# Optimization experiments

Measured on AMD Instinct MI355X. Metric: run time of the kernel, lower is better.

The kernel has to match this reference:

```python
import jax, jax.numpy as jnp
import numpy as np

H = 16
D_MODEL = 1024
D_K = D_MODEL // H  # 64
TEMP = float(np.sqrt(D_K))


def setup_inputs() -> dict:
    key = jax.random.key(0)
    ks = jax.random.split(key, 12)
    N = 2048
    s_in = 1.0 / np.sqrt(D_MODEL)
    inp = {
        "query": jax.random.normal(ks[0], (N, D_MODEL), jnp.float32),
        "key": jax.random.normal(ks[1], (N, D_MODEL), jnp.float32),
        "value": jax.random.normal(ks[2], (N, D_MODEL), jnp.float32),
        "Wq": jax.random.normal(ks[3], (D_MODEL, D_MODEL), jnp.float32) * s_in,
        "bq": jnp.zeros((D_MODEL,), jnp.float32),
        "Wk": jax.random.normal(ks[4], (D_MODEL, D_MODEL), jnp.float32) * s_in,
        "bk": jnp.zeros((D_MODEL,), jnp.float32),
        "Wv": jax.random.normal(ks[5], (D_MODEL, D_MODEL), jnp.float32) * s_in,
        "bv": jnp.zeros((D_MODEL,), jnp.float32),
        "Wo": jax.random.normal(ks[6], (D_MODEL, D_MODEL), jnp.float32) * s_in,
        "bo": jnp.zeros((D_MODEL,), jnp.float32),
    }
    return inp


def reference(query, key, value, Wq, bq, Wk, bk, Wv, bv, Wo, bo):
    # Project then split heads exactly like view(-1, h, d_k).transpose(0, 1):
    # (N, d_model) -> (N, h, d_k) -> (h, N, d_k)
    q = (query @ Wq + bq).reshape(-1, H, D_K).transpose(1, 0, 2)
    k = (key @ Wk + bk).reshape(-1, H, D_K).transpose(1, 0, 2)
    v = (value @ Wv + bv).reshape(-1, H, D_K).transpose(1, 0, 2)
    # Scaled dot-product attention (dropout is inference-mode identity)
    scores = jnp.einsum("hnd,hmd->hnm", q / TEMP, k)  # (h, N, N)
    attn = jax.nn.softmax(scores, axis=-1)
    x = jnp.einsum("hnm,hmd->hnd", attn, v)  # (h, N, d_k)
    x = x.transpose(1, 0, 2).reshape(-1, H * D_K)  # (N, d_model)
    out = x @ Wo + bo
    return (out, attn)
```

## Files before the change

### kernel.cpp

```cpp
#include <hip/hip_runtime.h>
#include <math.h>

#define NTOK 2048
#define DMODEL 1024
#define NHEAD 16
#define DHEAD 64
#define NTIL (NTOK / 64)

typedef _Float16 f16x8 __attribute__((ext_vector_type(8)));
typedef _Float16 f16x4 __attribute__((ext_vector_type(4)));
typedef _Float16 f16x2 __attribute__((ext_vector_type(2)));
typedef float f32x4 __attribute__((ext_vector_type(4)));
typedef float f32x16 __attribute__((ext_vector_type(16)));

union U32H2 { f16x2 h; unsigned u; };
union U8 { f16x8 v; unsigned u[4]; };

__device__ __forceinline__ void split16(float x, _Float16& hi, _Float16& lo) {
    hi = (_Float16)x;
    lo = (_Float16)(x - (float)hi);
}
__device__ __forceinline__ unsigned packh(_Float16 a, _Float16 b) {
    U32H2 c; c.h = f16x2{a, b}; return c.u;
}

__global__ void __launch_bounds__(256) prep_w_kernel(
        const float* __restrict__ Wq, const float* __restrict__ Wk,
        const float* __restrict__ Wv, const float* __restrict__ Wo,
        _Float16* __restrict__ Wt) {
    __shared__ float T[32][33];
    const int z = blockIdx.z;
    const float* W = (z == 0) ? Wq : (z == 1) ? Wk : (z == 2) ? Wv : Wo;
    _Float16* Whi = Wt + (size_t)z * 2 * 1024 * 1024;
    _Float16* Wlo = Whi + (size_t)1024 * 1024;
    const int t = threadIdx.x;
    const int k0 = blockIdx.y * 32, n0 = blockIdx.x * 32;
    const int r = t >> 3, c4 = (t & 7) * 4;
    const float4 v = *(const float4*)(W + (size_t)(k0 + r) * DMODEL + n0 + c4);
    T[r][c4 + 0] = v.x; T[r][c4 + 1] = v.y; T[r][c4 + 2] = v.z; T[r][c4 + 3] = v.w;
    __syncthreads();
    f16x4 hv, lv;
#pragma unroll
    for (int j = 0; j < 4; ++j) {
        _Float16 h, l;
        split16(T[c4 + j][r], h, l);
        hv[j] = h; lv[j] = l;
    }
    *(f16x4*)(Whi + (size_t)(n0 + r) * DMODEL + k0 + c4) = hv;
    *(f16x4*)(Wlo + (size_t)(n0 + r) * DMODEL + k0 + c4) = lv;
}

__global__ void __launch_bounds__(256) prep_a_kernel(
        const float* __restrict__ q, const float* __restrict__ k, const float* __restrict__ v,
        _Float16* __restrict__ As) {
    const int z = blockIdx.y;
    const float* A = (z == 0) ? q : (z == 1) ? k : v;
    const size_t PL = (size_t)NTOK * DMODEL;
    _Float16* H = As + (size_t)z * 2 * PL;
    _Float16* L = H + PL;
    const size_t off = ((size_t)blockIdx.x * 256 + threadIdx.x) * 8;
    const float4 a = *(const float4*)(A + off);
    const float4 b = *(const float4*)(A + off + 4);
    f16x8 hv, lv; _Float16 h, lo;
    split16(a.x, h, lo); hv[0] = h; lv[0] = lo;
    split16(a.y, h, lo); hv[1] = h; lv[1] = lo;
    split16(a.z, h, lo); hv[2] = h; lv[2] = lo;
    split16(a.w, h, lo); hv[3] = h; lv[3] = lo;
    split16(b.x, h, lo); hv[4] = h; lv[4] = lo;
    split16(b.y, h, lo); hv[5] = h; lv[5] = lo;
    split16(b.z, h, lo); hv[6] = h; lv[6] = lo;
    split16(b.w, h, lo); hv[7] = h; lv[7] = lo;
    *(f16x8*)(H + off) = hv;
    *(f16x8*)(L + off) = lv;
}

__global__ void __launch_bounds__(256) qkv_mfma_kernel(
        const _Float16* __restrict__ As,
        const _Float16* __restrict__ Wt,
        const float* __restrict__ bq, const float* __restrict__ bk, const float* __restrict__ bv,
        _Float16* __restrict__ Qh, _Float16* __restrict__ Ql,
        _Float16* __restrict__ Kh, _Float16* __restrict__ Vth) {
    __shared__ _Float16 Ah[64][40], Al[64][40], Bh[128][40], Bl[128][40];
    const int z = blockIdx.z;
    const size_t PL = (size_t)NTOK * DMODEL;
    const _Float16* AH = As + (size_t)z * 2 * PL;
    const _Float16* AL = AH + PL;
    const _Float16* WH = Wt + (size_t)z * 2 * 1024 * 1024;
    const _Float16* WL = WH + (size_t)1024 * 1024;
    const float* bias = (z == 0) ? bq : (z == 1) ? bk : bv;

    const int t = threadIdx.x;
    const int l = t & 63, wid = t >> 6;
    const int lr = l & 15, lk = l >> 4;
    const int m0 = blockIdx.y * 64, n0 = blockIdx.x * 128;
    const int wm = (wid >> 1) * 32, wn = (wid & 1) * 64;

    f32x4 acc[2][4];
#pragma unroll
    for (int mi = 0; mi < 2; ++mi)
#pragma unroll
        for (int ni = 0; ni < 4; ++ni)
#pragma unroll
            for (int e = 0; e < 4; ++e) acc[mi][ni][e] = 0.f;

    for (int k0 = 0; k0 < DMODEL; k0 += 32) {
        __syncthreads();
        {
            const int r = t >> 2, c8 = (t & 3) * 8;
            *(f16x8*)&Ah[r][c8] = *(const f16x8*)(AH + (size_t)(m0 + r) * DMODEL + k0 + c8);
            *(f16x8*)&Al[r][c8] = *(const f16x8*)(AL + (size_t)(m0 + r) * DMODEL + k0 + c8);
        }
#pragma unroll
        for (int p = 0; p < 2; ++p) {
            const int idx = t + p * 256;
            const int r = idx >> 2, c8 = (idx & 3) * 8;
            *(f16x8*)&Bh[r][c8] = *(const f16x8*)(WH + (size_t)(n0 + r) * DMODEL + k0 + c8);
            *(f16x8*)&Bl[r][c8] = *(const f16x8*)(WL + (size_t)(n0 + r) * DMODEL + k0 + c8);
        }
        __syncthreads();

        f16x8 ah[2], al[2], bh[4], bl[4];
#pragma unroll
        for (int i = 0; i < 2; ++i) {
            ah[i] = *(f16x8*)&Ah[wm + i * 16 + lr][lk * 8];
            al[i] = *(f16x8*)&Al[wm + i * 16 + lr][lk * 8];
        }
#pragma unroll
        for (int i = 0; i < 4; ++i) {
            bh[i] = *(f16x8*)&Bh[wn + i * 16 + lr][lk * 8];
            bl[i] = *(f16x8*)&Bl[wn + i * 16 + lr][lk * 8];
        }
        __builtin_amdgcn_s_setprio(1);
#pragma unroll
        for (int mi = 0; mi < 2; ++mi)
#pragma unroll
            for (int ni = 0; ni < 4; ++ni) {
                acc[mi][ni] = __builtin_amdgcn_mfma_f32_16x16x32_f16(ah[mi], bh[ni], acc[mi][ni], 0, 0, 0);
                acc[mi][ni] = __builtin_amdgcn_mfma_f32_16x16x32_f16(ah[mi], bl[ni], acc[mi][ni], 0, 0, 0);
                acc[mi][ni] = __builtin_amdgcn_mfma_f32_16x16x32_f16(al[mi], bh[ni], acc[mi][ni], 0, 0, 0);
            }
        __builtin_amdgcn_s_setprio(0);
    }

#pragma unroll
    for (int ni = 0; ni < 4; ++ni) {
        const int col = n0 + wn + ni * 16 + lr;
        const float bv_ = bias[col];
#pragma unroll
        for (int mi = 0; mi < 2; ++mi) {
            if (z == 2) {
                f16x4 hv;
#pragma unroll
                for (int i = 0; i < 4; ++i) hv[i] = (_Float16)(acc[mi][ni][i] + bv_);
                const int row = m0 + wm + mi * 16 + lk * 4;
                *(f16x4*)(Vth + (size_t)col * NTOK + row) = hv;
            } else {
#pragma unroll
                for (int i = 0; i < 4; ++i) {
                    const int row = m0 + wm + mi * 16 + lk * 4 + i;
                    float v = acc[mi][ni][i] + bv_;
                    if (z == 0) {
                        v *= 0.125f;
                        _Float16 h, lo;
                        split16(v, h, lo);
                        Qh[(size_t)row * DMODEL + col] = h;
                        Ql[(size_t)row * DMODEL + col] = lo;
                    } else {
                        Kh[(size_t)row * DMODEL + col] = (_Float16)v;
                    }
                }
            }
        }
    }
}

__global__ void __launch_bounds__(256, 2) fused_attn_kernel(
        const _Float16* __restrict__ Qh, const _Float16* __restrict__ Ql,
        const _Float16* __restrict__ Kh, const _Float16* __restrict__ Vth,
        float* __restrict__ attn, float* __restrict__ Xp) {
    __shared__ _Float16 KB[2][64][64];
    __shared__ _Float16 VB[2][64][64];
    const int t = threadIdx.x, l = t & 63, w = t >> 6, q = l & 31, h = l >> 5;
    const int hh = blockIdx.y;
    const int rw = blockIdx.x * 128 + w * 32;
    const int sr = t >> 3, sc = t & 7;
    const int qrow = rw + q;

    f16x8 qbh[4], qbl[4];
#pragma unroll
    for (int s = 0; s < 4; ++s) {
        const size_t off = (size_t)qrow * DMODEL + hh * DHEAD + s * 16 + h * 8;
        qbh[s] = *(const f16x8*)(Qh + off);
        qbl[s] = *(const f16x8*)(Ql + off);
    }

    auto stageK = [&](int buf, int j0) {
#pragma unroll
        for (int p = 0; p < 2; ++p) {
            const int r = sr + p * 32; const int cs = (sc ^ (r & 7)) * 8;
            *(f16x8*)&KB[buf][r][cs] = *(const f16x8*)(Kh + (size_t)(j0 + r) * DMODEL + hh * DHEAD + sc * 8);
        }
    };
    auto stageKV = [&](int buf, int j0) {
#pragma unroll
        for (int p = 0; p < 2; ++p) {
            const int r = sr + p * 32; const int cs = (sc ^ (r & 7)) * 8;
            *(f16x8*)&KB[buf][r][cs] = *(const f16x8*)(Kh + (size_t)(j0 + r) * DMODEL + hh * DHEAD + sc * 8);
            *(f16x8*)&VB[buf][r][cs] = *(const f16x8*)(Vth + (size_t)(hh * DHEAD + r) * NTOK + j0 + sc * 8);
        }
    };

    float lsum = 0.f;
    stageK(0, 0);
    for (int it = 0; it < NTIL; ++it) {
        __syncthreads();
        const int cur = it & 1;
        if (it + 1 < NTIL) stageK(cur ^ 1, (it + 1) * 64);
#pragma unroll
        for (int kb = 0; kb < 2; ++kb) {
            f32x16 c;
#pragma unroll
            for (int r = 0; r < 16; ++r) c[r] = 0.f;
            __builtin_amdgcn_s_setprio(1);
#pragma unroll
            for (int s = 0; s < 4; ++s) {
                const int rk = kb * 32 + q; const int cc = ((2 * s + h) ^ (rk & 7)) * 8;
                const f16x8 ah = *(f16x8*)&KB[cur][rk][cc];
                c = __builtin_amdgcn_mfma_f32_32x32x16_f16(ah, qbh[s], c, 0, 0, 0);
                c = __builtin_amdgcn_mfma_f32_32x32x16_f16(ah, qbl[s], c, 0, 0, 0);
            }
            __builtin_amdgcn_s_setprio(0);
#pragma unroll
            for (int r = 0; r < 16; ++r) lsum += __expf(c[r]);
        }
    }
    lsum += __shfl_xor(lsum, 32);
    const float linv = 1.f / lsum;

    f32x16 x0, x1;
#pragma unroll
    for (int r = 0; r < 16; ++r) { x0[r] = 0.f; x1[r] = 0.f; }

    __syncthreads();
    stageKV(0, 0);
    for (int it = 0; it < NTIL; ++it) {
        const int j0 = it * 64;
        __syncthreads();
        const int cur = it & 1;
        if (it + 1 < NTIL) stageKV(cur ^ 1, (it + 1) * 64);

#pragma unroll
        for (int kb = 0; kb < 2; ++kb) {
            f32x16 c;
#pragma unroll
            for (int r = 0; r < 16; ++r) c[r] = 0.f;
            __builtin_amdgcn_s_setprio(1);
#pragma unroll
            for (int s = 0; s < 4; ++s) {
                const int rk = kb * 32 + q; const int cc = ((2 * s + h) ^ (rk & 7)) * 8;
                const f16x8 ah = *(f16x8*)&KB[cur][rk][cc];
                c = __builtin_amdgcn_mfma_f32_32x32x16_f16(ah, qbh[s], c, 0, 0, 0);
                c = __builtin_amdgcn_mfma_f32_32x32x16_f16(ah, qbl[s], c, 0, 0, 0);
            }
            __builtin_amdgcn_s_setprio(0);

            float p[16];
#pragma unroll
            for (int r = 0; r < 16; ++r) p[r] = __expf(c[r]) * linv;

            const int kbase = j0 + kb * 32;
#pragma unroll
            for (int i = 0; i < 4; ++i) {
                f32x4 st;
                st[0] = p[4 * i]; st[1] = p[4 * i + 1]; st[2] = p[4 * i + 2]; st[3] = p[4 * i + 3];
                *(f32x4*)(attn + ((size_t)hh * NTOK + qrow) * NTOK + kbase + 8 * i + 4 * h) = st;
            }

            _Float16 hf[16];
#pragma unroll
            for (int r = 0; r < 16; ++r) hf[r] = (_Float16)p[r];
            unsigned ph[8];
#pragma unroll
            for (int i = 0; i < 8; ++i) ph[i] = packh(hf[2 * i], hf[2 * i + 1]);

#pragma unroll
            for (int ss = 0; ss < 2; ++ss) {
                const int b = 4 * ss;
                const unsigned eh0 = __shfl_xor(h ? ph[b + 0] : ph[b + 2], 32);
                const unsigned eh1 = __shfl_xor(h ? ph[b + 1] : ph[b + 3], 32);
                U8 pah;
                pah.u[0] = h ? eh0 : ph[b + 0]; pah.u[1] = h ? eh1 : ph[b + 1];
                pah.u[2] = h ? ph[b + 2] : eh0; pah.u[3] = h ? ph[b + 3] : eh1;
                const int ks = kb * 2 + ss;
                __builtin_amdgcn_s_setprio(1);
                {
                    const int rd0 = q; const int cv0 = ((2 * ks + h) ^ (rd0 & 7)) * 8;
                    const f16x8 vh = *(f16x8*)&VB[cur][rd0][cv0];
                    x0 = __builtin_amdgcn_mfma_f32_32x32x16_f16(pah.v, vh, x0, 0, 0, 0);
                }
                {
                    const int rd1 = 32 + q; const int cv1 = ((2 * ks + h) ^ (rd1 & 7)) * 8;
                    const f16x8 vh = *(f16x8*)&VB[cur][rd1][cv1];
                    x1 = __builtin_amdgcn_mfma_f32_32x32x16_f16(pah.v, vh, x1, 0, 0, 0);
                }
                __builtin_amdgcn_s_setprio(0);
            }
        }
    }

#pragma unroll
    for (int r = 0; r < 16; ++r) {
        const int qloc = (r & 3) + 8 * (r >> 2) + 4 * h;
        Xp[(size_t)(rw + qloc) * DMODEL + hh * DHEAD + q]      = x0[r];
        Xp[(size_t)(rw + qloc) * DMODEL + hh * DHEAD + 32 + q] = x1[r];
    }
}

__global__ void __launch_bounds__(256) out_mfma_kernel(
        const float* __restrict__ Xp,
        const _Float16* __restrict__ WH, const _Float16* __restrict__ WL,
        const float* __restrict__ bo, float* __restrict__ out) {
    __shared__ _Float16 Ah[64][40], Al[64][40], Bh[128][40], Bl[128][40];
    const int t = threadIdx.x;
    const int l = t & 63, wid = t >> 6;
    const int lr = l & 15, lk = l >> 4;
    const int m0 = blockIdx.y * 64, n0 = blockIdx.x * 128;
    const int wm = (wid >> 1) * 32, wn = (wid & 1) * 64;

    f32x4 acc[2][4];
#pragma unroll
    for (int mi = 0; mi < 2; ++mi)
#pragma unroll
        for (int ni = 0; ni < 4; ++ni)
#pragma unroll
            for (int e = 0; e < 4; ++e) acc[mi][ni][e] = 0.f;

    for (int k0 = 0; k0 < DMODEL; k0 += 32) {
        __syncthreads();
#pragma unroll
        for (int p = 0; p < 2; ++p) {
            const int idx = t + p * 256;
            const int r = idx >> 3, c4 = (idx & 7) * 4;
            const size_t off = (size_t)(m0 + r) * DMODEL + k0 + c4;
            const float4 v0 = *(const float4*)(Xp + off);
            f16x4 hv, lv; _Float16 h, lo;
            split16(v0.x, h, lo); hv[0] = h; lv[0] = lo;
            split16(v0.y, h, lo); hv[1] = h; lv[1] = lo;
            split16(v0.z, h, lo); hv[2] = h; lv[2] = lo;
            split16(v0.w, h, lo); hv[3] = h; lv[3] = lo;
            *(f16x4*)&Ah[r][c4] = hv;
            *(f16x4*)&Al[r][c4] = lv;
        }
#pragma unroll
        for (int p = 0; p < 2; ++p) {
            const int idx = t + p * 256;
            const int r = idx >> 2, c8 = (idx & 3) * 8;
            *(f16x8*)&Bh[r][c8] = *(const f16x8*)(WH + (size_t)(n0 + r) * DMODEL + k0 + c8);
            *(f16x8*)&Bl[r][c8] = *(const f16x8*)(WL + (size_t)(n0 + r) * DMODEL + k0 + c8);
        }
        __syncthreads();

        f16x8 ah[2], al[2], bh[4], bl[4];
#pragma unroll
        for (int i = 0; i < 2; ++i) {
            ah[i] = *(f16x8*)&Ah[wm + i * 16 + lr][lk * 8];
            al[i] = *(f16x8*)&Al[wm + i * 16 + lr][lk * 8];
        }
#pragma unroll
        for (int i = 0; i < 4; ++i) {
            bh[i] = *(f16x8*)&Bh[wn + i * 16 + lr][lk * 8];
            bl[i] = *(f16x8*)&Bl[wn + i * 16 + lr][lk * 8];
        }
        __builtin_amdgcn_s_setprio(1);
#pragma unroll
        for (int mi = 0; mi < 2; ++mi)
#pragma unroll
            for (int ni = 0; ni < 4; ++ni) {
                acc[mi][ni] = __builtin_amdgcn_mfma_f32_16x16x32_f16(ah[mi], bh[ni], acc[mi][ni], 0, 0, 0);
                acc[mi][ni] = __builtin_amdgcn_mfma_f32_16x16x32_f16(ah[mi], bl[ni], acc[mi][ni], 0, 0, 0);
                acc[mi][ni] = __builtin_amdgcn_mfma_f32_16x16x32_f16(al[mi], bh[ni], acc[mi][ni], 0, 0, 0);
            }
        __builtin_amdgcn_s_setprio(0);
    }

#pragma unroll
    for (int ni = 0; ni < 4; ++ni) {
        const int col = n0 + wn + ni * 16 + lr;
        const float bv_ = bo[col];
#pragma unroll
        for (int mi = 0; mi < 2; ++mi)
#pragma unroll
            for (int i = 0; i < 4; ++i) {
                const int row = m0 + wm + mi * 16 + lk * 4 + i;
                out[(size_t)row * DMODEL + col] = acc[mi][ni][i] + bv_;
            }
    }
}

extern "C" void kernel_launch(void* const* d_in, const int* in_sizes, int n_in,
                              void* d_out, int out_size, void* d_ws, size_t ws_size,
                              hipStream_t stream) {
    (void)in_sizes; (void)n_in; (void)out_size; (void)ws_size;
    const float* query = (const float*)d_in[0];
    const float* key_  = (const float*)d_in[1];
    const float* value = (const float*)d_in[2];
    const float* Wq = (const float*)d_in[3];
    const float* bq = (const float*)d_in[4];
    const float* Wk = (const float*)d_in[5];
    const float* bk = (const float*)d_in[6];
    const float* Wv = (const float*)d_in[7];
    const float* bv = (const float*)d_in[8];
    const float* Wo = (const float*)d_in[9];
    const float* bo = (const float*)d_in[10];

    float* out  = (float*)d_out;
    float* attn = out + (size_t)NTOK * DMODEL;

    const size_t MM = (size_t)1024 * 1024;
    _Float16* ws16 = (_Float16*)d_ws;
    _Float16* Wt  = ws16;
    _Float16* Qh  = ws16 + 8 * MM;
    _Float16* Ql  = Qh  + 2 * MM;
    _Float16* Kh_ = Ql  + 2 * MM;
    _Float16* Vth = Kh_ + 2 * MM;

    float* Xp = (float*)ws16;

    _Float16* As = (_Float16*)attn;

    dim3 blk(256);
    prep_w_kernel<<<dim3(32, 32, 4), blk, 0, stream>>>(Wq, Wk, Wv, Wo, Wt);
    prep_a_kernel<<<dim3(1024, 3), blk, 0, stream>>>(query, key_, value, As);
    qkv_mfma_kernel<<<dim3(8, 32, 3), blk, 0, stream>>>(As, Wt, bq, bk, bv,
                                                        Qh, Ql, Kh_, Vth);
    fused_attn_kernel<<<dim3(16, 16), blk, 0, stream>>>(Qh, Ql, Kh_, Vth, attn, Xp);
    out_mfma_kernel<<<dim3(8, 32), blk, 0, stream>>>(Xp, Wt + 6 * MM, Wt + 7 * MM, bo, out);
}
```

Before: 217.8 us.

## Split attention PV loop over two key halves and sum partials in output GEMM

The fused attention kernel's second pass (P·V accumulation) now covers only half of the key tiles per block, with a new grid z dimension of 2, and each half writes its partial output to a separate buffer. The output projection kernel loads both partial buffers and adds them before the fp16 hi/lo split. This doubles the block count from 256 to 512 so the GPU's compute units are better filled. The cost is that the first pass (row-sum over all keys) is still computed in full by both halves, plus extra partial-buffer writes and reads.

```diff
diff --git a/kernel.cpp b/kernel.cpp
--- a/kernel.cpp
+++ b/kernel.cpp
@@ -6,6 +6,7 @@
 #define NHEAD 16
 #define DHEAD 64
 #define NTIL (NTOK / 64)
+#define CTIL (NTIL / 2)
 
 typedef _Float16 f16x8 __attribute__((ext_vector_type(8)));
 typedef _Float16 f16x4 __attribute__((ext_vector_type(4)));
@@ -177,11 +178,11 @@
 __global__ void __launch_bounds__(256, 2) fused_attn_kernel(
         const _Float16* __restrict__ Qh, const _Float16* __restrict__ Ql,
         const _Float16* __restrict__ Kh, const _Float16* __restrict__ Vth,
-        float* __restrict__ attn, float* __restrict__ Xp) {
+        float* __restrict__ attn, float* __restrict__ Xp0, float* __restrict__ Xp1) {
     __shared__ _Float16 KB[2][64][64];
     __shared__ _Float16 VB[2][64][64];
     const int t = threadIdx.x, l = t & 63, w = t >> 6, q = l & 31, h = l >> 5;
-    const int hh = blockIdx.y;
+    const int hh = blockIdx.y, z = blockIdx.z;
     const int rw = blockIdx.x * 128 + w * 32;
     const int sr = t >> 3, sc = t & 7;
     const int qrow = rw + q;
@@ -241,13 +242,14 @@
 #pragma unroll
     for (int r = 0; r < 16; ++r) { x0[r] = 0.f; x1[r] = 0.f; }
 
+    const int jbase = z * CTIL * 64;
     __syncthreads();
-    stageKV(0, 0);
-    for (int it = 0; it < NTIL; ++it) {
-        const int j0 = it * 64;
+    stageKV(0, jbase);
+    for (int it = 0; it < CTIL; ++it) {
+        const int j0 = jbase + it * 64;
         __syncthreads();
         const int cur = it & 1;
-        if (it + 1 < NTIL) stageKV(cur ^ 1, (it + 1) * 64);
+        if (it + 1 < CTIL) stageKV(cur ^ 1, jbase + (it + 1) * 64);
 
 #pragma unroll
         for (int kb = 0; kb < 2; ++kb) {
@@ -308,16 +310,17 @@
         }
     }
 
+    float* __restrict__ Xout = z ? Xp1 : Xp0;
 #pragma unroll
     for (int r = 0; r < 16; ++r) {
         const int qloc = (r & 3) + 8 * (r >> 2) + 4 * h;
-        Xp[(size_t)(rw + qloc) * DMODEL + hh * DHEAD + q]      = x0[r];
-        Xp[(size_t)(rw + qloc) * DMODEL + hh * DHEAD + 32 + q] = x1[r];
+        Xout[(size_t)(rw + qloc) * DMODEL + hh * DHEAD + q]      = x0[r];
+        Xout[(size_t)(rw + qloc) * DMODEL + hh * DHEAD + 32 + q] = x1[r];
     }
 }
 
 __global__ void __launch_bounds__(256) out_mfma_kernel(
-        const float* __restrict__ Xp,
+        const float* __restrict__ Xp0, const float* __restrict__ Xp1,
         const _Float16* __restrict__ WH, const _Float16* __restrict__ WL,
         const float* __restrict__ bo, float* __restrict__ out) {
     __shared__ _Float16 Ah[64][40], Al[64][40], Bh[128][40], Bl[128][40];
@@ -342,12 +345,13 @@
             const int idx = t + p * 256;
             const int r = idx >> 3, c4 = (idx & 7) * 4;
             const size_t off = (size_t)(m0 + r) * DMODEL + k0 + c4;
-            const float4 v0 = *(const float4*)(Xp + off);
+            const float4 v0 = *(const float4*)(Xp0 + off);
+            const float4 v1 = *(const float4*)(Xp1 + off);
             f16x4 hv, lv; _Float16 h, lo;
-            split16(v0.x, h, lo); hv[0] = h; lv[0] = lo;
-            split16(v0.y, h, lo); hv[1] = h; lv[1] = lo;
-            split16(v0.z, h, lo); hv[2] = h; lv[2] = lo;
-            split16(v0.w, h, lo); hv[3] = h; lv[3] = lo;
+            split16(v0.x + v1.x, h, lo); hv[0] = h; lv[0] = lo;
+            split16(v0.y + v1.y, h, lo); hv[1] = h; lv[1] = lo;
+            split16(v0.z + v1.z, h, lo); hv[2] = h; lv[2] = lo;
+            split16(v0.w + v1.w, h, lo); hv[3] = h; lv[3] = lo;
             *(f16x4*)&Ah[r][c4] = hv;
             *(f16x4*)&Al[r][c4] = lv;
         }
@@ -424,7 +428,8 @@
     _Float16* Kh_ = Ql  + 2 * MM;
     _Float16* Vth = Kh_ + 2 * MM;
 
-    float* Xp = (float*)ws16;
+    float* Xp0 = (float*)ws16;
+    float* Xp1 = (float*)(ws16 + 20 * MM);
 
     _Float16* As = (_Float16*)attn;
 
@@ -433,6 +438,6 @@
     prep_a_kernel<<<dim3(1024, 3), blk, 0, stream>>>(query, key_, value, As);
     qkv_mfma_kernel<<<dim3(8, 32, 3), blk, 0, stream>>>(As, Wt, bq, bk, bv,
                                                         Qh, Ql, Kh_, Vth);
-    fused_attn_kernel<<<dim3(16, 16), blk, 0, stream>>>(Qh, Ql, Kh_, Vth, attn, Xp);
-    out_mfma_kernel<<<dim3(8, 32), blk, 0, stream>>>(Xp, Wt + 6 * MM, Wt + 7 * MM, bo, out);
-}
+    fused_attn_kernel<<<dim3(16, 16, 2), blk, 0, stream>>>(Qh, Ql, Kh_, Vth, attn, Xp0, Xp1);
+    out_mfma_kernel<<<dim3(8, 32), blk, 0, stream>>>(Xp0, Xp1, Wt + 6 * MM, Wt + 7 * MM, bo, out);
+}
```

Result: slower. 232.9 us (+6.9%).
